# Optimization experiments

Hardware: AMD Instinct MI355X
Metric: run time of the kernel (lower is better)

The kernel has to match this reference:

```python
import jax, jax.numpy as jnp
import numpy as np

B, N, K, F, OUT = 32, 2000, 32, 64, 128

def setup_inputs() -> dict:
    key = jax.random.key(0)
    k1, k2, k3, k4, k5 = jax.random.split(key, 5)
    x = jax.random.normal(k1, (B, N, F), dtype=jnp.float32)
    neighborhood = jax.random.randint(k2, (N, K), 0, N, dtype=jnp.int64)
    distances = jax.random.uniform(k3, (N, K), dtype=jnp.float32)
    # Linear(k*(F+1), OUT): torch default init scale ~ 1/sqrt(fan_in)
    fan_in = K * (F + 1)
    W = jax.random.normal(k4, (OUT, fan_in), dtype=jnp.float32) / np.sqrt(fan_in)
    b = jax.random.normal(k5, (OUT,), dtype=jnp.float32) / np.sqrt(fan_in)
    return {"x": x, "neighborhood": neighborhood, "distances": distances, "W": W, "b": b}

def reference(x, neighborhood, distances, W, b):
    batch, seq_len, feat = x.shape          # [B, N, F]
    k = neighborhood.shape[1]
    gathered = x[:, neighborhood, :]        # [B, N, K, F] gather over sequence dim
    d = jnp.broadcast_to(distances[None, :, :, None], (batch, seq_len, k, 1))
    h = jnp.concatenate([gathered, d], axis=-1)        # [B, N, K, F+1]
    h = h.reshape(batch, seq_len, k * (feat + 1))      # [B, N, K*(F+1)]
    out = jnp.einsum('bnf,of->bno', h, W) + b          # [B, N, OUT]
    return out
```

## Files before the change

### kernel.cpp

```cpp
#include <hip/hip_runtime.h>
#include <hip/hip_bf16.h>
#include <stdint.h>

typedef __attribute__((ext_vector_type(8)))  __bf16   bf16x8;
typedef __attribute__((ext_vector_type(4)))  float    f32x4;
typedef __attribute__((ext_vector_type(8)))  float    f32x8;

#define NN   2000
#define NK   32
#define NOUT 128

#define GLOBAL_AS __attribute__((address_space(1)))
#define LDS_AS    __attribute__((address_space(3)))
#define SB() __builtin_amdgcn_sched_barrier(0)
#define MFMA16 __builtin_amdgcn_mfma_f32_16x16x32_bf16

__global__ void kprep(const float* __restrict__ x, const float* __restrict__ dist,
                      const float* __restrict__ W,
                      __bf16* __restrict__ xb2h, __bf16* __restrict__ db,
                      __bf16* __restrict__ Wf2) {
  const int t = threadIdx.x;
  if (blockIdx.x < NN) {
    const int n = blockIdx.x;
    const int b  = t >> 3;
    const int f0 = (t & 7) << 3;
    const float* src = x + ((size_t)b * NN + n) * 64 + f0;
    f32x8 v = *(const f32x8*)src;
    bf16x8 r;
#pragma unroll
    for (int j = 0; j < 8; ++j) r[j] = (__bf16)v[j];
    const int h = b >> 4, row = b & 15;
    const int off = ((f0 >> 5) << 10) + (((((f0 >> 3) & 3) << 4) + row) << 4);
    *(bf16x8*)((char*)xb2h + ((size_t)(h * NN + n) << 11) + off) = r;
    if (t < NK) db[n * NK + t] = (__bf16)dist[n * NK + t];
  } else {
    const int kstep = blockIdx.x - NN;
#pragma unroll
    for (int pass = 0; pass < 2; ++pass) {
      const int it = t + pass * 256;
      const int og = it >> 6, lane = it & 63;
      const int o  = og * 16 + (lane & 15);
      const int kb = kstep * 32 + ((lane >> 4) << 3);
      bf16x8 r;
#pragma unroll
      for (int j = 0; j < 8; ++j) {
        const int kg = kb + j;
        const int col = (kg < 2048) ? ((kg >> 6) * 65 + (kg & 63)) : ((kg - 2048) * 65 + 64);
        r[j] = (__bf16)W[(size_t)o * 2080 + col];
      }
      *(bf16x8*)((char*)Wf2 + (size_t)kstep * 8192 + og * 1024 + lane * 16) = r;
    }
  }
}

__global__ __launch_bounds__(256, 2) void kmain(
    const int* __restrict__ nbrs, const float* __restrict__ bias,
    const __bf16* __restrict__ xb2h, const __bf16* __restrict__ Wf2,
    const __bf16* __restrict__ db, float* __restrict__ out) {
  __shared__ __align__(16) char lds[2][16384];

  const int t    = threadIdx.x;
  const int lane = t & 63;
  const int w    = t >> 6;
  const int h    = blockIdx.x & 1;
  const int n0   = (blockIdx.x >> 1) * 8 + w * 2;
  const int colo = lane & 15;
  const int rgrp = lane >> 4;

  f32x4 acc[2][8] = {};

  const int myidx = nbrs[(n0 + (lane >> 5)) * NK + (lane & 31)];

  const char* xb = (const char*)xb2h + ((size_t)(h * NN) << 11);
  const char* wf = (const char*)Wf2;

  auto loadA = [&](bf16x8 (*A)[2], int c) {
#pragma unroll
    for (int np = 0; np < 2; ++np) {
      const int nb = __builtin_amdgcn_readlane(myidx, np * 32 + c);
      const char* g = xb + ((size_t)nb << 11) + lane * 16;
      A[np][0] = *(const bf16x8*)(g);
      A[np][1] = *(const bf16x8*)(g + 1024);
    }
  };

  auto stageB = [&](int c) {
    const char* g = wf + ((size_t)c << 14) + (w << 12) + lane * 16;
    char* l = &lds[c & 1][w << 12];
#pragma unroll
    for (int q = 0; q < 4; ++q)
      __builtin_amdgcn_global_load_lds(
          (const GLOBAL_AS uint32_t*)(g + (q << 10)),
          (LDS_AS uint32_t*)(l + (q << 10)), 16, 0, 0);
  };

  auto compute = [&](int c, bf16x8 (*A)[2]) {
    const char* lb = &lds[c & 1][lane * 16];
    __builtin_amdgcn_s_setprio(1);
#pragma unroll
    for (int ks = 0; ks < 2; ++ks) {
#pragma unroll
      for (int og = 0; og < 8; ++og) {
        bf16x8 bf = *(const bf16x8*)(lb + (ks << 13) + (og << 10));
        acc[0][og] = MFMA16(A[0][ks], bf, acc[0][og], 0, 0, 0);
        acc[1][og] = MFMA16(A[1][ks], bf, acc[1][og], 0, 0, 0);
      }
    }
    __builtin_amdgcn_s_setprio(0);
  };

  bf16x8 A0[2][2], A1[2][2];

  loadA(A0, 0); SB();
  stageB(0); SB();

#define BODY(C, AC, AL)                                     \
  loadA(AL, (C) + 1); SB();                                 \
  asm volatile("s_waitcnt vmcnt(4)" ::: "memory");          \
  __builtin_amdgcn_s_barrier(); SB();                       \
  compute((C), AC); SB();                                   \
  stageB((C) + 1); SB();

  for (int c = 0; c < 30; c += 2) {
    BODY(c + 0, A0, A1)
    BODY(c + 1, A1, A0)
  }
  BODY(30, A0, A1)
#undef BODY
  asm volatile("s_waitcnt vmcnt(0)" ::: "memory");
  __builtin_amdgcn_s_barrier(); SB();
  compute(31, A1);

  {
    const char* wt = wf + ((size_t)64 << 13) + lane * 16;
    bf16x8 d0 = *(const bf16x8*)((const char*)db + (size_t)(n0 + 0) * 64 + (rgrp << 4));
    bf16x8 d1 = *(const bf16x8*)((const char*)db + (size_t)(n0 + 1) * 64 + (rgrp << 4));
#pragma unroll
    for (int og = 0; og < 8; ++og) {
      bf16x8 bf = *(const bf16x8*)(wt + (og << 10));
      acc[0][og] = MFMA16(d0, bf, acc[0][og], 0, 0, 0);
      acc[1][og] = MFMA16(d1, bf, acc[1][og], 0, 0, 0);
    }
  }

#pragma unroll
  for (int og = 0; og < 8; ++og) {
    const int o = (og << 4) + colo;
    const float bv = bias[o];
#pragma unroll
    for (int r = 0; r < 4; ++r) {
      const int b = (h << 4) + (rgrp << 2) + r;
      float* op = out + ((size_t)b * NN + n0) * NOUT + o;
      op[0]    = acc[0][og][r] + bv;
      op[NOUT] = acc[1][og][r] + bv;
    }
  }
}

extern "C" void kernel_launch(void* const* d_in, const int* in_sizes, int n_in,
                              void* d_out, int out_size, void* d_ws, size_t ws_size,
                              hipStream_t stream) {
  const float* x    = (const float*)d_in[0];
  const int*   nbrs = (const int*)d_in[1];
  const float* dist = (const float*)d_in[2];
  const float* W    = (const float*)d_in[3];
  const float* bias = (const float*)d_in[4];
  float* out = (float*)d_out;

  char* ws = (char*)d_ws;
  __bf16* xb2h = (__bf16*)(ws);
  __bf16* Wf2  = (__bf16*)(ws + 8192000);
  __bf16* db   = (__bf16*)(ws + 8192000 + 532480);

  kprep<<<NN + 65, 256, 0, stream>>>(x, dist, W, xb2h, db, Wf2);
  kmain<<<(NN / 8) * 2, 256, 0, stream>>>(nbrs, bias, xb2h, Wf2, db, out);
}
```

Before: 53.75 us.

## Deepen main loop pipeline to triple-buffered LDS and four A register sets

Changes the main GEMM loop from double-buffered W staging with one-chunk-ahead A prefetch to a triple-buffered LDS ring plus four register sets of gathered A tiles. Loads are issued two to three chunks ahead and the loop is fully unrolled with explicit vmcnt waits. The goal is to hide more global and gather latency behind the MFMA work. In exchange it uses more LDS (48KB per block) and more VGPRs, which may reduce occupancy under the launch bounds of two blocks per SIMD group.

```diff
diff --git a/kernel.cpp b/kernel.cpp
--- a/kernel.cpp
+++ b/kernel.cpp
@@ -57,7 +57,7 @@
     const int* __restrict__ nbrs, const float* __restrict__ bias,
     const __bf16* __restrict__ xb2h, const __bf16* __restrict__ Wf2,
     const __bf16* __restrict__ db, float* __restrict__ out) {
-  __shared__ __align__(16) char lds[2][16384];
+  __shared__ __align__(16) char lds[3][16384];
 
   const int t    = threadIdx.x;
   const int lane = t & 63;
@@ -84,9 +84,9 @@
     }
   };
 
-  auto stageB = [&](int c) {
+  auto stageB = [&](int buf, int c) {
     const char* g = wf + ((size_t)c << 14) + (w << 12) + lane * 16;
-    char* l = &lds[c & 1][w << 12];
+    char* l = &lds[buf][w << 12];
 #pragma unroll
     for (int q = 0; q < 4; ++q)
       __builtin_amdgcn_global_load_lds(
@@ -94,8 +94,8 @@
           (LDS_AS uint32_t*)(l + (q << 10)), 16, 0, 0);
   };
 
-  auto compute = [&](int c, bf16x8 (*A)[2]) {
-    const char* lb = &lds[c & 1][lane * 16];
+  auto compute = [&](int buf, bf16x8 (*A)[2]) {
+    const char* lb = &lds[buf][lane * 16];
     __builtin_amdgcn_s_setprio(1);
 #pragma unroll
     for (int ks = 0; ks < 2; ++ks) {
@@ -109,27 +109,43 @@
     __builtin_amdgcn_s_setprio(0);
   };
 
-  bf16x8 A0[2][2], A1[2][2];
+  bf16x8 A0[2][2], A1[2][2], A2[2][2], A3[2][2];
 
   loadA(A0, 0); SB();
-  stageB(0); SB();
+  stageB(0, 0); SB();
+  loadA(A1, 1); SB();
+  stageB(1, 1); SB();
+  loadA(A2, 2); SB();
 
-#define BODY(C, AC, AL)                                     \
-  loadA(AL, (C) + 1); SB();                                 \
-  asm volatile("s_waitcnt vmcnt(4)" ::: "memory");          \
+#define BODY(C, ACUR, ALD, BUFC, BUFS)                      \
+  asm volatile("s_waitcnt vmcnt(12)" ::: "memory");         \
   __builtin_amdgcn_s_barrier(); SB();                       \
-  compute((C), AC); SB();                                   \
-  stageB((C) + 1); SB();
+  stageB(BUFS, (C) + 2); SB();                              \
+  loadA(ALD, (C) + 3); SB();                                \
+  compute(BUFC, ACUR); SB();
 
-  for (int c = 0; c < 30; c += 2) {
-    BODY(c + 0, A0, A1)
-    BODY(c + 1, A1, A0)
-  }
-  BODY(30, A0, A1)
+  BODY( 0, A0, A3, 0, 2)  BODY( 1, A1, A0, 1, 0)  BODY( 2, A2, A1, 2, 1)
+  BODY( 3, A3, A2, 0, 2)  BODY( 4, A0, A3, 1, 0)  BODY( 5, A1, A0, 2, 1)
+  BODY( 6, A2, A1, 0, 2)  BODY( 7, A3, A2, 1, 0)  BODY( 8, A0, A3, 2, 1)
+  BODY( 9, A1, A0, 0, 2)  BODY(10, A2, A1, 1, 0)  BODY(11, A3, A2, 2, 1)
+  BODY(12, A0, A3, 0, 2)  BODY(13, A1, A0, 1, 0)  BODY(14, A2, A1, 2, 1)
+  BODY(15, A3, A2, 0, 2)  BODY(16, A0, A3, 1, 0)  BODY(17, A1, A0, 2, 1)
+  BODY(18, A2, A1, 0, 2)  BODY(19, A3, A2, 1, 0)  BODY(20, A0, A3, 2, 1)
+  BODY(21, A1, A0, 0, 2)  BODY(22, A2, A1, 1, 0)  BODY(23, A3, A2, 2, 1)
+  BODY(24, A0, A3, 0, 2)  BODY(25, A1, A0, 1, 0)  BODY(26, A2, A1, 2, 1)
+  BODY(27, A3, A2, 0, 2)  BODY(28, A0, A3, 1, 0)
 #undef BODY
+
+  asm volatile("s_waitcnt vmcnt(12)" ::: "memory");
+  __builtin_amdgcn_s_barrier(); SB();
+  stageB(1, 31); SB();
+  compute(2, A1); SB();
+  asm volatile("s_waitcnt vmcnt(8)" ::: "memory");
+  __builtin_amdgcn_s_barrier(); SB();
+  compute(0, A2); SB();
   asm volatile("s_waitcnt vmcnt(0)" ::: "memory");
   __builtin_amdgcn_s_barrier(); SB();
-  compute(31, A1);
+  compute(1, A3);
 
   {
     const char* wt = wf + ((size_t)64 << 13) + lane * 16;
```

New measurement: 52.43 us (median of 2 runs). -2.4%, faster.

## Give each wave four nodes, halve block size, triple-buffer weight staging

Applied to the files above, without the earlier changes.

Each wave now handles four sequence positions instead of two, so every LDS weight fragment feeds four MFMAs, and blocks shrink to two waves of 128 threads. Weight staging becomes a three-deep LDS ring that prefetches two chunks ahead, and the main loop is fully unrolled. This is meant to cut LDS reads and barrier overhead per unit of MFMA work and to hide weight-load latency better. The cost is twice the accumulator and A-fragment registers per wave, which may lower occupancy, plus fewer waves per block to hide gather latency.

```diff
diff --git a/kernel.cpp b/kernel.cpp
--- a/kernel.cpp
+++ b/kernel.cpp
@@ -53,49 +53,51 @@
   }
 }
 
-__global__ __launch_bounds__(256, 2) void kmain(
+__global__ __launch_bounds__(128) void kmain(
     const int* __restrict__ nbrs, const float* __restrict__ bias,
     const __bf16* __restrict__ xb2h, const __bf16* __restrict__ Wf2,
     const __bf16* __restrict__ db, float* __restrict__ out) {
-  __shared__ __align__(16) char lds[2][16384];
+  __shared__ __align__(16) char lds[3][16384];
 
   const int t    = threadIdx.x;
   const int lane = t & 63;
   const int w    = t >> 6;
   const int h    = blockIdx.x & 1;
-  const int n0   = (blockIdx.x >> 1) * 8 + w * 2;
+  const int n0   = (blockIdx.x >> 1) * 8 + w * 4;
   const int colo = lane & 15;
   const int rgrp = lane >> 4;
 
-  f32x4 acc[2][8] = {};
+  f32x4 acc[4][8] = {};
 
-  const int myidx = nbrs[(n0 + (lane >> 5)) * NK + (lane & 31)];
+  const int idxA = nbrs[(n0 + (lane >> 5)) * NK + (lane & 31)];
+  const int idxB = nbrs[(n0 + 2 + (lane >> 5)) * NK + (lane & 31)];
 
   const char* xb = (const char*)xb2h + ((size_t)(h * NN) << 11);
   const char* wf = (const char*)Wf2;
 
   auto loadA = [&](bf16x8 (*A)[2], int c) {
 #pragma unroll
-    for (int np = 0; np < 2; ++np) {
-      const int nb = __builtin_amdgcn_readlane(myidx, np * 32 + c);
+    for (int np = 0; np < 4; ++np) {
+      const int nb = __builtin_amdgcn_readlane((np < 2) ? idxA : idxB,
+                                               (np & 1) * 32 + c);
       const char* g = xb + ((size_t)nb << 11) + lane * 16;
       A[np][0] = *(const bf16x8*)(g);
       A[np][1] = *(const bf16x8*)(g + 1024);
     }
   };
 
-  auto stageB = [&](int c) {
-    const char* g = wf + ((size_t)c << 14) + (w << 12) + lane * 16;
-    char* l = &lds[c & 1][w << 12];
+  auto stageB = [&](int buf, int c) {
+    const char* g = wf + ((size_t)c << 14) + t * 16;
+    char* l = &lds[buf][t * 16];
 #pragma unroll
-    for (int q = 0; q < 4; ++q)
+    for (int q = 0; q < 8; ++q)
       __builtin_amdgcn_global_load_lds(
-          (const GLOBAL_AS uint32_t*)(g + (q << 10)),
-          (LDS_AS uint32_t*)(l + (q << 10)), 16, 0, 0);
+          (const GLOBAL_AS uint32_t*)(g + (q << 11)),
+          (LDS_AS uint32_t*)(l + (q << 11)), 16, 0, 0);
   };
 
-  auto compute = [&](int c, bf16x8 (*A)[2]) {
-    const char* lb = &lds[c & 1][lane * 16];
+  auto compute = [&](int buf, bf16x8 (*A)[2]) {
+    const char* lb = &lds[buf][lane * 16];
     __builtin_amdgcn_s_setprio(1);
 #pragma unroll
     for (int ks = 0; ks < 2; ++ks) {
@@ -104,42 +106,59 @@
         bf16x8 bf = *(const bf16x8*)(lb + (ks << 13) + (og << 10));
         acc[0][og] = MFMA16(A[0][ks], bf, acc[0][og], 0, 0, 0);
         acc[1][og] = MFMA16(A[1][ks], bf, acc[1][og], 0, 0, 0);
+        acc[2][og] = MFMA16(A[2][ks], bf, acc[2][og], 0, 0, 0);
+        acc[3][og] = MFMA16(A[3][ks], bf, acc[3][og], 0, 0, 0);
       }
     }
     __builtin_amdgcn_s_setprio(0);
   };
 
-  bf16x8 A0[2][2], A1[2][2];
+  bf16x8 A0[4][2], A1[4][2];
 
   loadA(A0, 0); SB();
-  stageB(0); SB();
+  stageB(0, 0); SB();
+  stageB(1, 1); SB();
 
-#define BODY(C, AC, AL)                                     \
+#define BODY(C, AC, AL, BUFC, BUFS)                         \
   loadA(AL, (C) + 1); SB();                                 \
-  asm volatile("s_waitcnt vmcnt(4)" ::: "memory");          \
+  asm volatile("s_waitcnt vmcnt(16)" ::: "memory");         \
   __builtin_amdgcn_s_barrier(); SB();                       \
-  compute((C), AC); SB();                                   \
-  stageB((C) + 1); SB();
+  stageB(BUFS, (C) + 2); SB();                              \
+  compute(BUFC, AC); SB();
 
-  for (int c = 0; c < 30; c += 2) {
-    BODY(c + 0, A0, A1)
-    BODY(c + 1, A1, A0)
-  }
-  BODY(30, A0, A1)
+  BODY( 0, A0, A1, 0, 2)  BODY( 1, A1, A0, 1, 0)  BODY( 2, A0, A1, 2, 1)
+  BODY( 3, A1, A0, 0, 2)  BODY( 4, A0, A1, 1, 0)  BODY( 5, A1, A0, 2, 1)
+  BODY( 6, A0, A1, 0, 2)  BODY( 7, A1, A0, 1, 0)  BODY( 8, A0, A1, 2, 1)
+  BODY( 9, A1, A0, 0, 2)  BODY(10, A0, A1, 1, 0)  BODY(11, A1, A0, 2, 1)
+  BODY(12, A0, A1, 0, 2)  BODY(13, A1, A0, 1, 0)  BODY(14, A0, A1, 2, 1)
+  BODY(15, A1, A0, 0, 2)  BODY(16, A0, A1, 1, 0)  BODY(17, A1, A0, 2, 1)
+  BODY(18, A0, A1, 0, 2)  BODY(19, A1, A0, 1, 0)  BODY(20, A0, A1, 2, 1)
+  BODY(21, A1, A0, 0, 2)  BODY(22, A0, A1, 1, 0)  BODY(23, A1, A0, 2, 1)
+  BODY(24, A0, A1, 0, 2)  BODY(25, A1, A0, 1, 0)  BODY(26, A0, A1, 2, 1)
+  BODY(27, A1, A0, 0, 2)  BODY(28, A0, A1, 1, 0)  BODY(29, A1, A0, 2, 1)
 #undef BODY
+
+  loadA(A1, 31); SB();
+  asm volatile("s_waitcnt vmcnt(16)" ::: "memory");
+  __builtin_amdgcn_s_barrier(); SB();
+  compute(0, A0); SB();
   asm volatile("s_waitcnt vmcnt(0)" ::: "memory");
   __builtin_amdgcn_s_barrier(); SB();
-  compute(31, A1);
+  compute(1, A1);
 
   {
     const char* wt = wf + ((size_t)64 << 13) + lane * 16;
     bf16x8 d0 = *(const bf16x8*)((const char*)db + (size_t)(n0 + 0) * 64 + (rgrp << 4));
     bf16x8 d1 = *(const bf16x8*)((const char*)db + (size_t)(n0 + 1) * 64 + (rgrp << 4));
+    bf16x8 d2 = *(const bf16x8*)((const char*)db + (size_t)(n0 + 2) * 64 + (rgrp << 4));
+    bf16x8 d3 = *(const bf16x8*)((const char*)db + (size_t)(n0 + 3) * 64 + (rgrp << 4));
 #pragma unroll
     for (int og = 0; og < 8; ++og) {
       bf16x8 bf = *(const bf16x8*)(wt + (og << 10));
       acc[0][og] = MFMA16(d0, bf, acc[0][og], 0, 0, 0);
       acc[1][og] = MFMA16(d1, bf, acc[1][og], 0, 0, 0);
+      acc[2][og] = MFMA16(d2, bf, acc[2][og], 0, 0, 0);
+      acc[3][og] = MFMA16(d3, bf, acc[3][og], 0, 0, 0);
     }
   }
 
@@ -151,8 +170,10 @@
     for (int r = 0; r < 4; ++r) {
       const int b = (h << 4) + (rgrp << 2) + r;
       float* op = out + ((size_t)b * NN + n0) * NOUT + o;
-      op[0]    = acc[0][og][r] + bv;
-      op[NOUT] = acc[1][og][r] + bv;
+      op[0 * NOUT] = acc[0][og][r] + bv;
+      op[1 * NOUT] = acc[1][og][r] + bv;
+      op[2 * NOUT] = acc[2][og][r] + bv;
+      op[3 * NOUT] = acc[3][og][r] + bv;
     }
   }
 }
@@ -173,5 +194,5 @@
   __bf16* db   = (__bf16*)(ws + 8192000 + 532480);
 
   kprep<<<NN + 65, 256, 0, stream>>>(x, dist, W, xb2h, db, Wf2);
-  kmain<<<(NN / 8) * 2, 256, 0, stream>>>(nbrs, bias, xb2h, Wf2, db, out);
+  kmain<<<(NN / 8) * 2, 128, 0, stream>>>(nbrs, bias, xb2h, Wf2, db, out);
 }
```

New measurement: 63.64 us. +18.4%, slower.

## Give each wave private double-buffered LDS weight tiles and drop block barriers

Applied to the files above, without the earlier changes.

Instead of the four waves cooperatively staging a shared 16 KB weight chunk and syncing with s_barrier each step, every wave now streams the full weight k-step into its own 8 KB LDS buffer. It keeps two buffers in flight, at a finer granularity of one k-slice per step with half the A loads each. This removes the per-iteration workgroup barrier and sched_barriers, so waves can run out of step with each other. In exchange each wave loads all weights itself, quadrupling weight traffic into LDS, and LDS use doubles to 64 KB per block. Correctness relies on hand-counted vmcnt waits.

```diff
diff --git a/kernel.cpp b/kernel.cpp
--- a/kernel.cpp
+++ b/kernel.cpp
@@ -12,7 +12,6 @@
 
 #define GLOBAL_AS __attribute__((address_space(1)))
 #define LDS_AS    __attribute__((address_space(3)))
-#define SB() __builtin_amdgcn_sched_barrier(0)
 #define MFMA16 __builtin_amdgcn_mfma_f32_16x16x32_bf16
 
 __global__ void kprep(const float* __restrict__ x, const float* __restrict__ dist,
@@ -57,7 +56,7 @@
     const int* __restrict__ nbrs, const float* __restrict__ bias,
     const __bf16* __restrict__ xb2h, const __bf16* __restrict__ Wf2,
     const __bf16* __restrict__ db, float* __restrict__ out) {
-  __shared__ __align__(16) char lds[2][16384];
+  __shared__ __align__(16) char lds[4][2][8192];
 
   const int t    = threadIdx.x;
   const int lane = t & 63;
@@ -74,70 +73,88 @@
   const char* xb = (const char*)xb2h + ((size_t)(h * NN) << 11);
   const char* wf = (const char*)Wf2;
 
-  auto loadA = [&](bf16x8 (*A)[2], int c) {
+  auto stageB = [&](int buf, int c) {
+    const char* g = wf + ((size_t)c << 13) + lane * 16;
+    char* l = &lds[w][buf][0];
 #pragma unroll
-    for (int np = 0; np < 2; ++np) {
-      const int nb = __builtin_amdgcn_readlane(myidx, np * 32 + c);
-      const char* g = xb + ((size_t)nb << 11) + lane * 16;
-      A[np][0] = *(const bf16x8*)(g);
-      A[np][1] = *(const bf16x8*)(g + 1024);
-    }
-  };
-
-  auto stageB = [&](int c) {
-    const char* g = wf + ((size_t)c << 14) + (w << 12) + lane * 16;
-    char* l = &lds[c & 1][w << 12];
-#pragma unroll
-    for (int q = 0; q < 4; ++q)
+    for (int q = 0; q < 8; ++q)
       __builtin_amdgcn_global_load_lds(
           (const GLOBAL_AS uint32_t*)(g + (q << 10)),
           (LDS_AS uint32_t*)(l + (q << 10)), 16, 0, 0);
   };
 
-  auto compute = [&](int c, bf16x8 (*A)[2]) {
-    const char* lb = &lds[c & 1][lane * 16];
-    __builtin_amdgcn_s_setprio(1);
+  auto loadA = [&](bf16x8* A, int c) {
 #pragma unroll
-    for (int ks = 0; ks < 2; ++ks) {
-#pragma unroll
-      for (int og = 0; og < 8; ++og) {
-        bf16x8 bf = *(const bf16x8*)(lb + (ks << 13) + (og << 10));
-        acc[0][og] = MFMA16(A[0][ks], bf, acc[0][og], 0, 0, 0);
-        acc[1][og] = MFMA16(A[1][ks], bf, acc[1][og], 0, 0, 0);
-      }
+    for (int np = 0; np < 2; ++np) {
+      const int nb = __builtin_amdgcn_readlane(myidx, np * 32 + (c >> 1));
+      A[np] = *(const bf16x8*)(xb + ((size_t)nb << 11) + ((c & 1) << 10) + lane * 16);
     }
-    __builtin_amdgcn_s_setprio(0);
   };
 
-  bf16x8 A0[2][2], A1[2][2];
+  bf16x8 A0[2], A1[2];
 
-  loadA(A0, 0); SB();
-  stageB(0); SB();
+  stageB(0, 0); loadA(A0, 0);
+  stageB(1, 1); loadA(A1, 1);
 
-#define BODY(C, AC, AL)                                     \
-  loadA(AL, (C) + 1); SB();                                 \
-  asm volatile("s_waitcnt vmcnt(4)" ::: "memory");          \
-  __builtin_amdgcn_s_barrier(); SB();                       \
-  compute((C), AC); SB();                                   \
-  stageB((C) + 1); SB();
+#define BODY(C, BUF, AC, LOAD_NEXT)                          \
+  {                                                          \
+    asm volatile("s_waitcnt vmcnt(10)" ::: "memory");        \
+    const char* lb = &lds[w][BUF][lane * 16];                \
+    bf16x8 bf0 = *(const bf16x8*)(lb);                       \
+    bf16x8 bf1 = *(const bf16x8*)(lb + 1024);                \
+    bf16x8 bf2 = *(const bf16x8*)(lb + 2048);                \
+    bf16x8 bf3 = *(const bf16x8*)(lb + 3072);                \
+    bf16x8 bf4 = *(const bf16x8*)(lb + 4096);                \
+    bf16x8 bf5 = *(const bf16x8*)(lb + 5120);                \
+    bf16x8 bf6 = *(const bf16x8*)(lb + 6144);                \
+    bf16x8 bf7 = *(const bf16x8*)(lb + 7168);                \
+    stageB(BUF, (C) + 2);                                    \
+    __builtin_amdgcn_s_setprio(1);                           \
+    acc[0][0] = MFMA16(AC[0], bf0, acc[0][0], 0, 0, 0);      \
+    acc[1][0] = MFMA16(AC[1], bf0, acc[1][0], 0, 0, 0);      \
+    acc[0][1] = MFMA16(AC[0], bf1, acc[0][1], 0, 0, 0);      \
+    acc[1][1] = MFMA16(AC[1], bf1, acc[1][1], 0, 0, 0);      \
+    acc[0][2] = MFMA16(AC[0], bf2, acc[0][2], 0, 0, 0);      \
+    acc[1][2] = MFMA16(AC[1], bf2, acc[1][2], 0, 0, 0);      \
+    acc[0][3] = MFMA16(AC[0], bf3, acc[0][3], 0, 0, 0);      \
+    acc[1][3] = MFMA16(AC[1], bf3, acc[1][3], 0, 0, 0);      \
+    acc[0][4] = MFMA16(AC[0], bf4, acc[0][4], 0, 0, 0);      \
+    acc[1][4] = MFMA16(AC[1], bf4, acc[1][4], 0, 0, 0);      \
+    acc[0][5] = MFMA16(AC[0], bf5, acc[0][5], 0, 0, 0);      \
+    acc[1][5] = MFMA16(AC[1], bf5, acc[1][5], 0, 0, 0);      \
+    acc[0][6] = MFMA16(AC[0], bf6, acc[0][6], 0, 0, 0);      \
+    acc[1][6] = MFMA16(AC[1], bf6, acc[1][6], 0, 0, 0);      \
+    acc[0][7] = MFMA16(AC[0], bf7, acc[0][7], 0, 0, 0);      \
+    acc[1][7] = MFMA16(AC[1], bf7, acc[1][7], 0, 0, 0);      \
+    __builtin_amdgcn_s_setprio(0);                           \
+    if (LOAD_NEXT) loadA(AC, (C) + 2);                       \
+  }
 
-  for (int c = 0; c < 30; c += 2) {
-    BODY(c + 0, A0, A1)
-    BODY(c + 1, A1, A0)
+  for (int c = 0; c < 62; c += 2) {
+    BODY(c + 0, 0, A0, 1)
+    BODY(c + 1, 1, A1, 1)
   }
-  BODY(30, A0, A1)
-#undef BODY
-  asm volatile("s_waitcnt vmcnt(0)" ::: "memory");
-  __builtin_amdgcn_s_barrier(); SB();
-  compute(31, A1);
-
+  BODY(62, 0, A0, 0)
   {
-    const char* wt = wf + ((size_t)64 << 13) + lane * 16;
+    asm volatile("s_waitcnt vmcnt(8)" ::: "memory");
+    const char* lb = &lds[w][1][lane * 16];
+    bf16x8 bfv[8];
+#pragma unroll
+    for (int og = 0; og < 8; ++og) bfv[og] = *(const bf16x8*)(lb + (og << 10));
+#pragma unroll
+    for (int og = 0; og < 8; ++og) {
+      acc[0][og] = MFMA16(A1[0], bfv[og], acc[0][og], 0, 0, 0);
+      acc[1][og] = MFMA16(A1[1], bfv[og], acc[1][og], 0, 0, 0);
+    }
+  }
+  {
+    asm volatile("s_waitcnt vmcnt(0)" ::: "memory");
+    const char* lb = &lds[w][0][lane * 16];
     bf16x8 d0 = *(const bf16x8*)((const char*)db + (size_t)(n0 + 0) * 64 + (rgrp << 4));
     bf16x8 d1 = *(const bf16x8*)((const char*)db + (size_t)(n0 + 1) * 64 + (rgrp << 4));
 #pragma unroll
     for (int og = 0; og < 8; ++og) {
-      bf16x8 bf = *(const bf16x8*)(wt + (og << 10));
+      bf16x8 bf = *(const bf16x8*)(lb + (og << 10));
       acc[0][og] = MFMA16(d0, bf, acc[0][og], 0, 0, 0);
       acc[1][og] = MFMA16(d1, bf, acc[1][og], 0, 0, 0);
     }
```

Measured after the change: 63.83 us. 18.8% more time.
